# Kernel tuning notes

Hardware: AMD Instinct MI355X
Metric: run time of the kernel (lower is better)

## Reference

```python
import jax, jax.numpy as jnp
import numpy as np

EPS = 1.1920929e-07  # torch.finfo(float32).eps, default for F.rms_norm
HQ, HKV = 16, 4
WIN = 256

def rmsnorm(x):
    return x * jax.lax.rsqrt(jnp.mean(x * x, axis=-1, keepdims=True) + EPS)

def setup_inputs() -> dict:
    key = jax.random.key(0)
    ks = jax.random.split(key, 5)
    B, T, C = 2, 2048, 2048
    Dh = C // HQ
    s = 0.02
    x = jax.random.normal(ks[0], (B, T, C), jnp.float32)
    Wq = jax.random.normal(ks[1], (C, HQ * Dh), jnp.float32) * s
    Wk = jax.random.normal(ks[2], (C, HKV * Dh), jnp.float32) * s
    Wv = jax.random.normal(ks[3], (C, HKV * Dh), jnp.float32) * s
    Wo = jax.random.normal(ks[4], (C, C), jnp.float32) * s
    return {"x": x, "Wq": Wq, "Wk": Wk, "Wv": Wv, "Wo": Wo}

def reference(x, Wq, Wk, Wv, Wo):
    B, T, C = x.shape
    Dh = C // HQ
    g = HQ // HKV
    # projections (Linear bias=False); weights stored [in,out]
    Q = (x @ Wq).reshape(B, T, HQ, Dh).transpose(0, 2, 1, 3)   # [B,Hq,T,Dh]
    V = (x @ Wv).reshape(B, T, HKV, Dh).transpose(0, 2, 1, 3)  # [B,Hkv,T,Dh]
    _K_unused = x @ Wk  # source computes c_k(x) but then overwrites K = norm(V)
    Q = rmsnorm(Q)
    K = rmsnorm(V)  # faithful to source bug: K = norm(V)
    Q = Q.reshape(B, HKV, g, T, Dh)
    scores = jnp.einsum('bhgtd,bhsd->bhgts', Q, K)  # no 1/sqrt(Dh) scale, as in source
    i = jnp.arange(T)[:, None]
    j = jnp.arange(T)[None, :]
    mask = (j > i) & (j <= i - WIN)
    scores = jnp.where(mask, -jnp.inf, scores)
    p = jax.nn.softmax(scores, axis=-1)
    y = jnp.einsum('bhgts,bhsd->bhgtd', p, V)
    y = y.reshape(B, HQ, T, Dh).transpose(0, 2, 1, 3).reshape(B, T, C)
    return rmsnorm(y @ Wo)
```

## Files before the change

kernel.cpp:

```cpp
#include <hip/hip_runtime.h>
#include <math.h>

#define BB   2
#define TT   2048
#define CC   2048
#define HQ_  16
#define HKV_ 4
#define DH   128
#define MM   (BB * TT)
#define KVC  (HKV_ * DH)

typedef __attribute__((ext_vector_type(8)))  _Float16 f16x8;
typedef __attribute__((ext_vector_type(4)))  float    f32x4;

__device__ __forceinline__ unsigned short f2h(float x) {
    _Float16 h = (_Float16)x;
    return __builtin_bit_cast(unsigned short, h);
}
__device__ __forceinline__ float h2f(unsigned short u) {
    return (float)__builtin_bit_cast(_Float16, u);
}
__device__ __forceinline__ void gll16(const void* g, void* l) {
    __builtin_amdgcn_global_load_lds(
        (const __attribute__((address_space(1))) unsigned int*)g,
        (__attribute__((address_space(3))) unsigned int*)l, 16, 0, 0);
}
__device__ __forceinline__ int xcd_swizzle(int lid, int nwg) {
    const int xcd = lid & 7, rank = lid >> 3;
    const int q8 = nwg >> 3, r8 = nwg & 7;
    return (xcd < r8 ? xcd * (q8 + 1) : r8 * (q8 + 1) + (xcd - r8) * q8) + rank;
}

__global__ __launch_bounds__(256)
void cast_f16(const float* __restrict__ in, unsigned short* __restrict__ out, int n8) {
    int i = blockIdx.x * blockDim.x + threadIdx.x;
    const int stride = gridDim.x * blockDim.x;
    for (; i < n8; i += stride) {
        const float4 a = ((const float4*)in)[i * 2 + 0];
        const float4 b = ((const float4*)in)[i * 2 + 1];
        uint4 o;
        o.x = (unsigned)f2h(a.x) | ((unsigned)f2h(a.y) << 16);
        o.y = (unsigned)f2h(a.z) | ((unsigned)f2h(a.w) << 16);
        o.z = (unsigned)f2h(b.x) | ((unsigned)f2h(b.y) << 16);
        o.w = (unsigned)f2h(b.z) | ((unsigned)f2h(b.w) << 16);
        ((uint4*)out)[i] = o;
    }
}

__global__ __launch_bounds__(256)
void tcast(const float* __restrict__ W, unsigned short* __restrict__ WT, int Kd, int Nd) {
    __shared__ float Ls[32][33];
    const int n0 = blockIdx.x * 32, k0 = blockIdx.y * 32;
    const int i = threadIdx.x;
    {
        const int kr = i >> 3, n4 = (i & 7) * 4;
        float4 v = *(const float4*)&W[(size_t)(k0 + kr) * Nd + n0 + n4];
        Ls[kr][n4 + 0] = v.x; Ls[kr][n4 + 1] = v.y;
        Ls[kr][n4 + 2] = v.z; Ls[kr][n4 + 3] = v.w;
    }
    __syncthreads();
    {
        const int nr = i >> 3, k4 = (i & 7) * 4;
        uint2 o;
        o.x = (unsigned)f2h(Ls[k4 + 0][nr]) | ((unsigned)f2h(Ls[k4 + 1][nr]) << 16);
        o.y = (unsigned)f2h(Ls[k4 + 2][nr]) | ((unsigned)f2h(Ls[k4 + 3][nr]) << 16);
        *(uint2*)&WT[(size_t)(n0 + nr) * Kd + k0 + k4] = o;
    }
}

template<int F16OUT>
__global__ __launch_bounds__(256)
void gemm_bt(const unsigned short* __restrict__ A, const unsigned short* __restrict__ Bt,
             void* __restrict__ Cout, int M, int N, int K) {
    __shared__ __align__(16) unsigned short As[128 * 64];
    __shared__ __align__(16) unsigned short Bs[128 * 64];
    const int tid  = threadIdx.x;
    const int lane = tid & 63, wid = tid >> 6;
    const int g = lane >> 4, l15 = lane & 15;
    const int nwg  = gridDim.x * gridDim.y;
    const int tile = xcd_swizzle(blockIdx.y * gridDim.x + blockIdx.x, nwg);
    const int bm = (tile / gridDim.x) * 128, bn = (tile % gridDim.x) * 128;
    const int wr = (wid >> 1) * 64, wc = (wid & 1) * 64;

    f32x4 acc[4][4] = {};

    for (int kt = 0; kt < K; kt += 64) {
        __syncthreads();
#pragma unroll
        for (int r = 0; r < 4; ++r) {
            const int q = r * 256 + tid;
            const int row = q >> 3, c = q & 7, sc = c ^ (row & 7);
            gll16(A + (size_t)(bm + row) * K + kt + sc * 8, As + q * 8);
        }
#pragma unroll
        for (int r = 0; r < 4; ++r) {
            const int q = r * 256 + tid;
            const int row = q >> 3, c = q & 7, sc = c ^ (row & 7);
            gll16(Bt + (size_t)(bn + row) * K + kt + sc * 8, Bs + q * 8);
        }
        __syncthreads();

#pragma unroll
        for (int kk = 0; kk < 2; ++kk) {
            f16x8 af[4], bfr[4];
#pragma unroll
            for (int m = 0; m < 4; ++m) {
                const int row = wr + m * 16 + l15;
                const int ch = (kk * 4 + g) ^ (row & 7);
                af[m] = *(const f16x8*)&As[row * 64 + ch * 8];
            }
#pragma unroll
            for (int n = 0; n < 4; ++n) {
                const int row = wc + n * 16 + l15;
                const int ch = (kk * 4 + g) ^ (row & 7);
                bfr[n] = *(const f16x8*)&Bs[row * 64 + ch * 8];
            }
#pragma unroll
            for (int m = 0; m < 4; ++m)
#pragma unroll
                for (int n = 0; n < 4; ++n)
                    acc[m][n] = __builtin_amdgcn_mfma_f32_16x16x32_f16(
                        af[m], bfr[n], acc[m][n], 0, 0, 0);
        }
    }

#pragma unroll
    for (int m = 0; m < 4; ++m)
#pragma unroll
        for (int n = 0; n < 4; ++n)
#pragma unroll
            for (int r = 0; r < 4; ++r) {
                const int row = bm + wr + m * 16 + g * 4 + r;
                const int col = bn + wc + n * 16 + l15;
                const float v = acc[m][n][r];
                if (F16OUT)
                    ((unsigned short*)Cout)[(size_t)row * N + col] = f2h(v);
                else
                    ((float*)Cout)[(size_t)row * N + col] = v;
            }
}

__global__ __launch_bounds__(256)
void rms128_h(const unsigned short* __restrict__ in, unsigned short* __restrict__ out,
              int nrows, float post) {
    const int row  = blockIdx.x * 4 + (threadIdx.x >> 6);
    const int lane = threadIdx.x & 63;
    if (row >= nrows) return;
    const unsigned u = *(const unsigned*)(in + (size_t)row * DH + lane * 2);
    const float a = h2f((unsigned short)(u & 0xffff));
    const float b = h2f((unsigned short)(u >> 16));
    float ss = a * a + b * b;
#pragma unroll
    for (int o = 32; o >= 1; o >>= 1) ss += __shfl_xor(ss, o);
    const float sc = rsqrtf(ss * (1.f / DH) + 1.1920929e-07f) * post;
    const unsigned ov = (unsigned)f2h(a * sc) | ((unsigned)f2h(b * sc) << 16);
    *(unsigned*)(out + (size_t)row * DH + lane * 2) = ov;
}

__global__ __launch_bounds__(256)
void vt_build(const unsigned short* __restrict__ Vg, unsigned short* __restrict__ Vt) {
    __shared__ unsigned short Ls[32][36];
    const int t0 = blockIdx.x * 32;
    const int d0 = blockIdx.y * 32;
    const int bh = blockIdx.z;
    const int b = bh >> 2, hk = bh & 3;
    const int i = threadIdx.x;
    {
        const int tr = i >> 3, d4 = (i & 7) * 4;
        const unsigned short* src = Vg + (size_t)(b * TT + t0 + tr) * KVC + hk * DH + d0 + d4;
        const unsigned u0 = *(const unsigned*)(src);
        const unsigned u1 = *(const unsigned*)(src + 2);
        Ls[tr][d4 + 0] = (unsigned short)(u0 & 0xffff);
        Ls[tr][d4 + 1] = (unsigned short)(u0 >> 16);
        Ls[tr][d4 + 2] = (unsigned short)(u1 & 0xffff);
        Ls[tr][d4 + 3] = (unsigned short)(u1 >> 16);
    }
    __syncthreads();
    {
        const int dr = i >> 3, t4 = (i & 7) * 4;
        unsigned short* dst = Vt + ((size_t)bh * DH + d0 + dr) * TT + t0 + t4;
        const unsigned o0 = (unsigned)Ls[t4 + 0][dr] | ((unsigned)Ls[t4 + 1][dr] << 16);
        const unsigned o1 = (unsigned)Ls[t4 + 2][dr] | ((unsigned)Ls[t4 + 3][dr] << 16);
        *(unsigned*)(dst)     = o0;
        *(unsigned*)(dst + 2) = o1;
    }
}

__global__ __launch_bounds__(256, 4)
void attn_mfma(const unsigned short* __restrict__ Qb, const unsigned short* __restrict__ Kb,
               const unsigned short* __restrict__ Vt, unsigned short* __restrict__ Yb) {
    __shared__ __align__(16) unsigned short Ks[2][32 * 128];
    __shared__ __align__(16) unsigned short Vs[2][128 * 32];
    __shared__ __align__(16) unsigned short Ps[4][16 * 32];

    const int tid  = threadIdx.x;
    const int lane = tid & 63, wid = tid >> 6;
    const int g = lane >> 4, l15 = lane & 15;
    const int q0 = blockIdx.x * 64;
    const int bh = blockIdx.y;
    const int b = bh >> 4, h = bh & 15, hk = h >> 2;

    const size_t kbase = (size_t)(b * TT) * KVC + hk * DH;
    const size_t vbase = (size_t)(b * HKV_ + hk) * DH * TT;

#define STAGE(buf, st)                                                         \
    do {                                                                       \
        _Pragma("unroll")                                                      \
        for (int r = 0; r < 2; ++r) {                                          \
            const int qq = r * 256 + tid;                                      \
            const int key = qq >> 4, c = qq & 15, sc = c ^ (key & 7);          \
            gll16(Kb + kbase + (size_t)((st) + key) * KVC + sc * 8,            \
                  &Ks[buf][qq * 8]);                                           \
        }                                                                      \
        _Pragma("unroll")                                                      \
        for (int r = 0; r < 2; ++r) {                                          \
            const int qq = r * 256 + tid;                                      \
            const int d = qq >> 2, c = qq & 3;                                 \
            const int sc = c ^ (d & 3) ^ ((d >> 2) & 3);                       \
            gll16(Vt + vbase + (size_t)d * TT + (st) + sc * 8,                 \
                  &Vs[buf][qq * 8]);                                           \
        }                                                                      \
    } while (0)

    STAGE(0, 0);

    f16x8 qf[4];
    {
        const unsigned short* qp =
            Qb + (size_t)(b * TT + q0 + wid * 16 + l15) * CC + h * DH + g * 8;
#pragma unroll
        for (int kk = 0; kk < 4; ++kk) qf[kk] = *(const f16x8*)(qp + kk * 32);
    }
    {
        float ss = 0.f;
#pragma unroll
        for (int kk = 0; kk < 4; ++kk)
#pragma unroll
            for (int j = 0; j < 8; ++j) { const float v = (float)qf[kk][j]; ss += v * v; }
        ss += __shfl_xor(ss, 16);
        ss += __shfl_xor(ss, 32);
        const float qsc = rsqrtf(ss * (1.f / DH) + 1.1920929e-07f) * 1.4426950408889634f;
#pragma unroll
        for (int kk = 0; kk < 4; ++kk)
#pragma unroll
            for (int j = 0; j < 8; ++j)
                qf[kk][j] = (_Float16)((float)qf[kk][j] * qsc);
    }

    f16x8 ones_b;
    {
        const _Float16 v = (l15 == 0) ? (_Float16)1.0f : (_Float16)0.0f;
#pragma unroll
        for (int j = 0; j < 8; ++j) ones_b[j] = v;
    }

    float mr[4];
    f32x4 acc[9] = {};
#pragma unroll
    for (int r = 0; r < 4; ++r) mr[r] = -3.0e38f;

    unsigned short* pw = Ps[wid];

    asm volatile("s_waitcnt vmcnt(0)" ::: "memory");
    __builtin_amdgcn_s_barrier();

    const int NT = TT / 32;
    for (int t = 0; t < NT; ++t) {
        const int cur = t & 1;
        if (t + 1 < NT) STAGE(cur ^ 1, (t + 1) * 32);

        const unsigned short* ksp = Ks[cur];
        const unsigned short* vsp = Vs[cur];

        f32x4 s[2] = {};
        __builtin_amdgcn_s_setprio(1);
#pragma unroll
        for (int kk = 0; kk < 4; ++kk)
#pragma unroll
            for (int n = 0; n < 2; ++n) {
                const int key = n * 16 + l15;
                const int ch = (kk * 4 + g) ^ (key & 7);
                const f16x8 kf = *(const f16x8*)&ksp[key * 128 + ch * 8];
                s[n] = __builtin_amdgcn_mfma_f32_16x16x32_f16(qf[kk], kf, s[n], 0, 0, 0);
            }
        __builtin_amdgcn_s_setprio(0);

        float m0[4];
        bool need = false;
#pragma unroll
        for (int r = 0; r < 4; ++r) {
            m0[r] = fmaxf(s[0][r], s[1][r]);
            need = need || (m0[r] > mr[r] + 8.f);
        }
        if (__any(need)) {
            float scale[4];
#pragma unroll
            for (int r = 0; r < 4; ++r) {
                float mx = m0[r];
#pragma unroll
                for (int o = 8; o >= 1; o >>= 1) mx = fmaxf(mx, __shfl_xor(mx, o));
                const float mn = fmaxf(mr[r], mx);
                scale[r] = __builtin_amdgcn_exp2f(mr[r] - mn);
                mr[r] = mn;
            }
#pragma unroll
            for (int f = 0; f < 9; ++f) {
                acc[f][0] *= scale[0]; acc[f][1] *= scale[1];
                acc[f][2] *= scale[2]; acc[f][3] *= scale[3];
            }
        }

#pragma unroll
        for (int n = 0; n < 2; ++n) {
            const int colc = n * 2 + (l15 >> 3);
            const int cel  = l15 & 7;
#pragma unroll
            for (int r = 0; r < 4; ++r) {
                const float p = __builtin_amdgcn_exp2f(s[n][r] - mr[r]);
                const int row = g * 4 + r;
                const int ch = colc ^ (row & 3) ^ g;
                pw[row * 32 + ch * 8 + cel] = f2h(p);
            }
        }

        __builtin_amdgcn_s_setprio(1);
        {
            const int ch = g ^ (l15 & 3) ^ ((l15 >> 2) & 3);
            const f16x8 pa = *(const f16x8*)&pw[l15 * 32 + ch * 8];
#pragma unroll
            for (int f = 0; f < 8; ++f) {
                const int dr = f * 16 + l15;
                const int vch = g ^ (dr & 3) ^ ((dr >> 2) & 3);
                const f16x8 vf = *(const f16x8*)&vsp[dr * 32 + vch * 8];
                acc[f] = __builtin_amdgcn_mfma_f32_16x16x32_f16(pa, vf, acc[f], 0, 0, 0);
            }
            acc[8] = __builtin_amdgcn_mfma_f32_16x16x32_f16(pa, ones_b, acc[8], 0, 0, 0);
        }
        __builtin_amdgcn_s_setprio(0);

        asm volatile("s_waitcnt vmcnt(0)" ::: "memory");
        __builtin_amdgcn_s_barrier();
    }
#undef STAGE

    float inv[4];
#pragma unroll
    for (int r = 0; r < 4; ++r) {
        const float l = __shfl(acc[8][r], lane & 48);
        inv[r] = 1.f / l;
    }
#pragma unroll
    for (int f = 0; f < 8; ++f)
#pragma unroll
        for (int r = 0; r < 4; ++r) {
            const int t = q0 + wid * 16 + g * 4 + r;
            const int col = h * DH + f * 16 + l15;
            Yb[(size_t)(b * TT + t) * CC + col] = f2h(acc[f][r] * inv[r]);
        }
}

__global__ __launch_bounds__(256)
void rms2048_h(const unsigned short* __restrict__ in, float* __restrict__ out) {
    __shared__ float red[4];
    const int tid = threadIdx.x;
    const unsigned short* p = in + (size_t)blockIdx.x * CC + tid * 8;
    const uint4 u = *(const uint4*)p;
    float v[8];
    v[0] = h2f((unsigned short)(u.x & 0xffff)); v[1] = h2f((unsigned short)(u.x >> 16));
    v[2] = h2f((unsigned short)(u.y & 0xffff)); v[3] = h2f((unsigned short)(u.y >> 16));
    v[4] = h2f((unsigned short)(u.z & 0xffff)); v[5] = h2f((unsigned short)(u.z >> 16));
    v[6] = h2f((unsigned short)(u.w & 0xffff)); v[7] = h2f((unsigned short)(u.w >> 16));
    float ss = 0.f;
#pragma unroll
    for (int j = 0; j < 8; ++j) ss += v[j] * v[j];
#pragma unroll
    for (int o = 32; o >= 1; o >>= 1) ss += __shfl_xor(ss, o);
    if ((tid & 63) == 0) red[tid >> 6] = ss;
    __syncthreads();
    const float tot = red[0] + red[1] + red[2] + red[3];
    const float sc = rsqrtf(tot * (1.f / CC) + 1.1920929e-07f);
    float* q = out + (size_t)blockIdx.x * CC + tid * 8;
    *(float4*)&q[0] = make_float4(v[0] * sc, v[1] * sc, v[2] * sc, v[3] * sc);
    *(float4*)&q[4] = make_float4(v[4] * sc, v[5] * sc, v[6] * sc, v[7] * sc);
}

extern "C" void kernel_launch(void* const* d_in, const int* in_sizes, int n_in,
                              void* d_out, int out_size, void* d_ws, size_t ws_size,
                              hipStream_t stream) {
    const float* x  = (const float*)d_in[0];
    const float* Wq = (const float*)d_in[1];
    const float* Wv = (const float*)d_in[3];
    const float* Wo = (const float*)d_in[4];
    float* out = (float*)d_out;

    char* ws = (char*)d_ws;
    const size_t MB = 1024 * 1024;
    unsigned short* xb  = (unsigned short*)(ws);
    unsigned short* WqT = (unsigned short*)(ws + 16 * MB);
    unsigned short* WoT = WqT;
    unsigned short* WvT = (unsigned short*)(ws + 24 * MB);
    unsigned short* Qg  = (unsigned short*)(ws + 26 * MB);
    unsigned short* Vg  = (unsigned short*)(ws + 42 * MB);
    unsigned short* Kb  = (unsigned short*)(ws + 46 * MB);
    unsigned short* Vt  = (unsigned short*)(ws + 50 * MB);
    unsigned short* Yb  = (unsigned short*)(ws + 54 * MB);

    const dim3 blk(256);

    cast_f16<<<2048, blk, 0, stream>>>(x, xb, MM * CC / 8);
    tcast<<<dim3(CC / 32, CC / 32), blk, 0, stream>>>(Wq, WqT, CC, CC);
    tcast<<<dim3(KVC / 32, CC / 32), blk, 0, stream>>>(Wv, WvT, CC, KVC);

    gemm_bt<1><<<dim3(CC / 128, MM / 128), blk, 0, stream>>>(xb, WqT, Qg, MM, CC, CC);
    gemm_bt<1><<<dim3(KVC / 128, MM / 128), blk, 0, stream>>>(xb, WvT, Vg, MM, KVC, CC);

    tcast<<<dim3(CC / 32, CC / 32), blk, 0, stream>>>(Wo, WoT, CC, CC);

    rms128_h<<<MM * HKV_ / 4, blk, 0, stream>>>(Vg, Kb, MM * HKV_, 1.f);
    vt_build<<<dim3(TT / 32, DH / 32, BB * HKV_), blk, 0, stream>>>(Vg, Vt);

    attn_mfma<<<dim3(TT / 64, BB * HQ_), blk, 0, stream>>>(Qg, Kb, Vt, Yb);

    gemm_bt<1><<<dim3(CC / 128, MM / 128), blk, 0, stream>>>(Yb, WoT, xb, MM, CC, CC);
    rms2048_h<<<MM, blk, 0, stream>>>(xb, out);
}
```

Measured before the change: 285.8 us.

## Merge Q and V projections into one GEMM and fuse K norm with V transpose

Concatenates the transposed Wq and Wv weights so one GEMM writes a combined [M, C+KVC] Q|V buffer, which replaces two launches and gives a larger grid (20x32 tiles). The separate rms128 and vt_build kernels are merged into one kvprep kernel. It reads each V row once, writes the normalized K and the transposed V from shared memory, and uses wider 16-byte accesses. Attention now reads Q with the wider row stride. The risk is that the combined output buffer must fit the workspace region, and the strided Q reads may be less cache friendly.

```diff
diff --git a/kernel.cpp b/kernel.cpp
--- a/kernel.cpp
+++ b/kernel.cpp
@@ -9,6 +9,7 @@
 #define DH   128
 #define MM   (BB * TT)
 #define KVC  (HKV_ * DH)
+#define QVN  (CC + KVC)
 
 typedef __attribute__((ext_vector_type(8)))  _Float16 f16x8;
 typedef __attribute__((ext_vector_type(4)))  float    f32x4;
@@ -141,48 +142,62 @@
 }
 
 __global__ __launch_bounds__(256)
-void rms128_h(const unsigned short* __restrict__ in, unsigned short* __restrict__ out,
-              int nrows, float post) {
-    const int row  = blockIdx.x * 4 + (threadIdx.x >> 6);
-    const int lane = threadIdx.x & 63;
-    if (row >= nrows) return;
-    const unsigned u = *(const unsigned*)(in + (size_t)row * DH + lane * 2);
-    const float a = h2f((unsigned short)(u & 0xffff));
-    const float b = h2f((unsigned short)(u >> 16));
-    float ss = a * a + b * b;
-#pragma unroll
-    for (int o = 32; o >= 1; o >>= 1) ss += __shfl_xor(ss, o);
-    const float sc = rsqrtf(ss * (1.f / DH) + 1.1920929e-07f) * post;
-    const unsigned ov = (unsigned)f2h(a * sc) | ((unsigned)f2h(b * sc) << 16);
-    *(unsigned*)(out + (size_t)row * DH + lane * 2) = ov;
-}
-
-__global__ __launch_bounds__(256)
-void vt_build(const unsigned short* __restrict__ Vg, unsigned short* __restrict__ Vt) {
-    __shared__ unsigned short Ls[32][36];
+void kvprep(const unsigned short* __restrict__ Vg,
+            unsigned short* __restrict__ Kb, unsigned short* __restrict__ Vt) {
+    __shared__ unsigned short Ls[32][132];
     const int t0 = blockIdx.x * 32;
-    const int d0 = blockIdx.y * 32;
-    const int bh = blockIdx.z;
+    const int bh = blockIdx.y;
     const int b = bh >> 2, hk = bh & 3;
-    const int i = threadIdx.x;
-    {
-        const int tr = i >> 3, d4 = (i & 7) * 4;
-        const unsigned short* src = Vg + (size_t)(b * TT + t0 + tr) * KVC + hk * DH + d0 + d4;
-        const unsigned u0 = *(const unsigned*)(src);
-        const unsigned u1 = *(const unsigned*)(src + 2);
-        Ls[tr][d4 + 0] = (unsigned short)(u0 & 0xffff);
-        Ls[tr][d4 + 1] = (unsigned short)(u0 >> 16);
-        Ls[tr][d4 + 2] = (unsigned short)(u1 & 0xffff);
-        Ls[tr][d4 + 3] = (unsigned short)(u1 >> 16);
+    const int tid = threadIdx.x;
+
+    const int tr = tid >> 3, c16 = (tid & 7) * 16;
+    const unsigned short* src =
+        Vg + (size_t)(b * TT + t0 + tr) * QVN + hk * DH + c16;
+    const uint4 u0 = *(const uint4*)(src);
+    const uint4 u1 = *(const uint4*)(src + 8);
+    *(uint4*)&Ls[tr][c16]     = u0;
+    *(uint4*)&Ls[tr][c16 + 8] = u1;
+
+    float v[16];
+    {
+        const unsigned uu[8] = {u0.x, u0.y, u0.z, u0.w, u1.x, u1.y, u1.z, u1.w};
+#pragma unroll
+        for (int j = 0; j < 8; ++j) {
+            v[2 * j]     = h2f((unsigned short)(uu[j] & 0xffff));
+            v[2 * j + 1] = h2f((unsigned short)(uu[j] >> 16));
+        }
+    }
+    float ss = 0.f;
+#pragma unroll
+    for (int j = 0; j < 16; ++j) ss += v[j] * v[j];
+    ss += __shfl_xor(ss, 1);
+    ss += __shfl_xor(ss, 2);
+    ss += __shfl_xor(ss, 4);
+    const float sc = rsqrtf(ss * (1.f / DH) + 1.1920929e-07f);
+
+    {
+        unsigned short* kd = Kb + (size_t)(b * TT + t0 + tr) * KVC + hk * DH + c16;
+        uint4 o0, o1;
+        unsigned oo[8];
+#pragma unroll
+        for (int j = 0; j < 8; ++j)
+            oo[j] = (unsigned)f2h(v[2 * j] * sc) | ((unsigned)f2h(v[2 * j + 1] * sc) << 16);
+        o0 = make_uint4(oo[0], oo[1], oo[2], oo[3]);
+        o1 = make_uint4(oo[4], oo[5], oo[6], oo[7]);
+        *(uint4*)(kd)     = o0;
+        *(uint4*)(kd + 8) = o1;
     }
     __syncthreads();
-    {
-        const int dr = i >> 3, t4 = (i & 7) * 4;
-        unsigned short* dst = Vt + ((size_t)bh * DH + d0 + dr) * TT + t0 + t4;
-        const unsigned o0 = (unsigned)Ls[t4 + 0][dr] | ((unsigned)Ls[t4 + 1][dr] << 16);
-        const unsigned o1 = (unsigned)Ls[t4 + 2][dr] | ((unsigned)Ls[t4 + 3][dr] << 16);
-        *(unsigned*)(dst)     = o0;
-        *(unsigned*)(dst + 2) = o1;
+
+    {
+        const int dr = tid >> 1, t16 = (tid & 1) * 16;
+        unsigned oo[8];
+#pragma unroll
+        for (int j = 0; j < 8; ++j)
+            oo[j] = (unsigned)Ls[t16 + 2 * j][dr] | ((unsigned)Ls[t16 + 2 * j + 1][dr] << 16);
+        unsigned short* dst = Vt + ((size_t)bh * DH + dr) * TT + t0 + t16;
+        *(uint4*)(dst)     = make_uint4(oo[0], oo[1], oo[2], oo[3]);
+        *(uint4*)(dst + 8) = make_uint4(oo[4], oo[5], oo[6], oo[7]);
     }
 }
 
@@ -227,7 +242,7 @@
     f16x8 qf[4];
     {
         const unsigned short* qp =
-            Qb + (size_t)(b * TT + q0 + wid * 16 + l15) * CC + h * DH + g * 8;
+            Qb + (size_t)(b * TT + q0 + wid * 16 + l15) * QVN + h * DH + g * 8;
 #pragma unroll
         for (int kk = 0; kk < 4; ++kk) qf[kk] = *(const f16x8*)(qp + kk * 32);
     }
@@ -395,31 +410,30 @@
 
     char* ws = (char*)d_ws;
     const size_t MB = 1024 * 1024;
-    unsigned short* xb  = (unsigned short*)(ws);
-    unsigned short* WqT = (unsigned short*)(ws + 16 * MB);
-    unsigned short* WoT = WqT;
-    unsigned short* WvT = (unsigned short*)(ws + 24 * MB);
-    unsigned short* Qg  = (unsigned short*)(ws + 26 * MB);
-    unsigned short* Vg  = (unsigned short*)(ws + 42 * MB);
-    unsigned short* Kb  = (unsigned short*)(ws + 46 * MB);
-    unsigned short* Vt  = (unsigned short*)(ws + 50 * MB);
-    unsigned short* Yb  = (unsigned short*)(ws + 54 * MB);
+    unsigned short* xb   = (unsigned short*)(ws);
+    unsigned short* WqvT = (unsigned short*)(ws + 16 * MB);
+    unsigned short* WoT  = WqvT;
+    unsigned short* QVg  = (unsigned short*)(ws + 26 * MB);
+    unsigned short* Kb   = (unsigned short*)(ws + 46 * MB);
+    unsigned short* Vt   = (unsigned short*)(ws + 50 * MB);
+    unsigned short* Yb   = (unsigned short*)(ws + 54 * MB);
+
+    const unsigned short* Qb = QVg;
+    const unsigned short* Vg = QVg + CC;
 
     const dim3 blk(256);
 
     cast_f16<<<2048, blk, 0, stream>>>(x, xb, MM * CC / 8);
-    tcast<<<dim3(CC / 32, CC / 32), blk, 0, stream>>>(Wq, WqT, CC, CC);
-    tcast<<<dim3(KVC / 32, CC / 32), blk, 0, stream>>>(Wv, WvT, CC, KVC);
-
-    gemm_bt<1><<<dim3(CC / 128, MM / 128), blk, 0, stream>>>(xb, WqT, Qg, MM, CC, CC);
-    gemm_bt<1><<<dim3(KVC / 128, MM / 128), blk, 0, stream>>>(xb, WvT, Vg, MM, KVC, CC);
+    tcast<<<dim3(CC / 32, CC / 32), blk, 0, stream>>>(Wq, WqvT, CC, CC);
+    tcast<<<dim3(KVC / 32, CC / 32), blk, 0, stream>>>(Wv, WqvT + (size_t)CC * CC, CC, KVC);
+
+    gemm_bt<1><<<dim3(QVN / 128, MM / 128), blk, 0, stream>>>(xb, WqvT, QVg, MM, QVN, CC);
 
     tcast<<<dim3(CC / 32, CC / 32), blk, 0, stream>>>(Wo, WoT, CC, CC);
 
-    rms128_h<<<MM * HKV_ / 4, blk, 0, stream>>>(Vg, Kb, MM * HKV_, 1.f);
-    vt_build<<<dim3(TT / 32, DH / 32, BB * HKV_), blk, 0, stream>>>(Vg, Vt);
-
-    attn_mfma<<<dim3(TT / 64, BB * HQ_), blk, 0, stream>>>(Qg, Kb, Vt, Yb);
+    kvprep<<<dim3(TT / 32, BB * HKV_), blk, 0, stream>>>(Vg, Kb, Vt);
+
+    attn_mfma<<<dim3(TT / 64, BB * HQ_), blk, 0, stream>>>(Qb, Kb, Vt, Yb);
 
     gemm_bt<1><<<dim3(CC / 128, MM / 128), blk, 0, stream>>>(Yb, WoT, xb, MM, CC, CC);
     rms2048_h<<<MM, blk, 0, stream>>>(xb, out);
```

Result: faster. 273.0 us (-4.5%).
